# Performance work log

Measured on AMD Instinct MI355X. Metric: run time of the kernel, lower is better.

Reference implementation:

```python
import jax, jax.numpy as jnp
import numpy as np

B, E, U, N = 2, 16, 8, 400
D = E + U  # GP input dim = obs_dim + action_dim


def _psd(key, b, n, scale):
    a = jax.random.normal(key, (b, n, n)) * scale
    return a @ jnp.swapaxes(a, -1, -2) + 1e-4 * jnp.eye(n, dtype=jnp.float32)


def setup_inputs() -> dict:
    key = jax.random.key(0)
    ks = jax.random.split(key, 9)
    X_train = jax.random.normal(ks[0], (N, D), dtype=jnp.float32)
    lengthscales = jax.random.uniform(ks[1], (E, D), minval=0.7, maxval=1.5, dtype=jnp.float32)
    variances = jax.random.uniform(ks[2], (E, 1), minval=0.5, maxval=1.5, dtype=jnp.float32)
    noises = jnp.full((E,), 0.01, dtype=jnp.float32)
    y_train = jax.random.normal(ks[3], (N, E), dtype=jnp.float32) * 0.1

    # cached factorizations, exactly as _extract_parameters builds them
    Xs = X_train[None] / lengthscales[:, None, :]                   # (E,N,D)
    sq = jnp.sum(Xs * Xs, -1)
    d2 = jnp.maximum(sq[:, :, None] + sq[:, None, :] - 2.0 * jnp.einsum('end,emd->enm', Xs, Xs), 0.0)
    K = variances[:, :, None] * jnp.exp(-0.5 * d2)
    K = K + (noises[:, None, None] + 1e-6) * jnp.eye(N, dtype=jnp.float32)
    L = jnp.linalg.cholesky(K)
    inv_K = jax.scipy.linalg.cho_solve((L, True), jnp.broadcast_to(jnp.eye(N, dtype=jnp.float32), (E, N, N)))
    beta = jax.scipy.linalg.cho_solve((L, True), y_train.T[:, :, None])[..., 0]  # (E,N)

    m_x = jax.random.normal(ks[4], (B, E), dtype=jnp.float32)
    m_u = jax.random.normal(ks[5], (B, U), dtype=jnp.float32)
    s_x = _psd(ks[6], B, E, 0.05)
    s_u = _psd(ks[7], B, U, 0.05)
    c_xu = jax.random.normal(ks[8], (B, E, U), dtype=jnp.float32) * 0.1
    return dict(m_x=m_x, s_x=s_x, m_u=m_u, s_u=s_u, c_xu=c_xu,
                X_train=X_train, lengthscales=lengthscales, variances=variances,
                noises=noises, inv_K=inv_K, beta=beta)


def _moment_match(m_x, s_x, m_u, s_u, c_xu, X_train, lengthscales, variances, noises, inv_K, beta):
    Eo = m_x.shape[-1]
    Din = X_train.shape[-1]
    m = jnp.concatenate([m_x, m_u], axis=-1)                        # (B,D) joint input mean
    s_c = s_x @ c_xu                                                # (B,E,U) joint cross block
    S = jnp.concatenate([
        jnp.concatenate([s_x, s_c], axis=-1),
        jnp.concatenate([jnp.swapaxes(s_c, -1, -2), s_u], axis=-1)], axis=-2)  # (B,D,D)

    inp = X_train[None] - m[:, None]                                # (B,N,D)  nu_n = x_n - m
    iL = 1.0 / lengthscales                                         # (E,D)  Lambda^{-1/2}
    iLsq = iL * iL                                                  # (E,D)  Lambda^{-1}
    eyeD = jnp.eye(Din, dtype=m_x.dtype)

    # ---- predictive mean: q_n = s2 |Bm|^{-1/2} exp(-0.5 nu Bm^{-1} nu),  Bm = L^{-1/2} S L^{-1/2} + I
    inv_N = inp[:, None] * iL[None, :, None]                        # (B,E,N,D)
    Bmat = iL[None, :, :, None] * S[:, None] * iL[None, :, None, :] + eyeD  # (B,E,D,D)
    t = jnp.swapaxes(jnp.linalg.solve(Bmat, jnp.swapaxes(inv_N, -1, -2)), -1, -2)  # (B,E,N,D)
    lb = jnp.exp(-0.5 * jnp.sum(inv_N * t, -1)) * beta[None]        # (B,E,N)
    _, logdetB = jnp.linalg.slogdet(Bmat)
    c = variances[:, 0][None] * jnp.exp(-0.5 * logdetB)             # (B,E)
    pred_mean = jnp.sum(lb, -1) * c                                 # (B,E)

    # ---- input-output covariance V (premultiplication by S applied below)
    t_iL = t * iL[None, :, None, :]                                 # rows: nu_n (Lambda + S)^{-1}
    V = jnp.einsum('bend,ben->bde', t_iL, lb) * c[:, None, :]       # (B,D,E)

    # ---- predictive covariance via exact moment matching (PILCO)
    z = inp[:, None] * iLsq[None, :, None]                          # (B,E,N,D) = nu Lambda_a^{-1}
    iLsum = iLsq[:, None] + iLsq[None]                              # (E,E,D)
    R = S[:, None, None] * iLsum[None, :, :, None, :] + eyeD        # (B,E,E,D,D)
    Q2 = 0.5 * jnp.linalg.solve(R, jnp.broadcast_to(S[:, None, None], R.shape))
    Xs = jnp.einsum('band,bacde,bane->bacn', z, Q2, z)              # (B,E,E,N)
    X2s = jnp.einsum('bcnd,bacde,bcne->bacn', z, Q2, z)
    cross = 2.0 * jnp.einsum('baid,bacde,bcje->bacij', z, Q2, z)    # (B,E,E,N,N)
    logk = jnp.log(variances[:, 0])[None, :, None] - 0.5 * jnp.einsum('bnd,ed->ben', inp * inp, iLsq)
    Lmat = jnp.exp(logk[:, :, None, :, None] + logk[:, None, :, None, :]
                   + Xs[..., :, None] + X2s[..., None, :] + cross)  # (B,E,E,N,N)
    _, logdetR = jnp.linalg.slogdet(R)
    scale = jnp.exp(-0.5 * logdetR)                                 # (B,E,E)
    S_bLb = jnp.einsum('ai,bacij,cj->bac', beta, Lmat, beta)
    diagL = Lmat[:, jnp.arange(Eo), jnp.arange(Eo)]                 # (B,E,N,N)
    tr = jnp.einsum('aij,baij->ba', inv_K, diagL)                   # tr(K^{-1} Q_aa)
    eyeE = jnp.eye(Eo, dtype=m_x.dtype)
    S_delta = (S_bLb - eyeE[None] * tr[:, :, None]) * scale \
              + eyeE[None] * variances[:, 0][None, :, None] \
              - pred_mean[:, :, None] * pred_mean[:, None, :]

    # GP predicts the residual delta: next = obs + delta
    next_mean = m_x + pred_mean
    Cx = S[:, :Eo, :] @ V                                           # cov(x, delta), (B,E,E)
    next_var = s_x + S_delta + Cx + jnp.swapaxes(Cx, -1, -2)
    return next_mean, next_var


def reference(m_x, s_x, m_u, s_u, c_xu, X_train, lengthscales, variances, noises, inv_K, beta):
    return _moment_match(m_x, s_x, m_u, s_u, c_xu, X_train, lengthscales, variances, noises, inv_K, beta)
```

## Files before the change

### kernel.cpp

```cpp
#include <hip/hip_runtime.h>
#include <math.h>

#define Bdim 2
#define Edim 16
#define Udim 8
#define Ndim 400
#define Ddim 24
#define NPAIR 136

#define WS_S     0
#define WS_INP   1152
#define WS_LOGK  20352
#define WS_PM    33152
#define WS_V     33184
#define WS_SBLB  33952
#define WS_TR    34464
#define WS_SCALE 34496

__global__ __launch_bounds__(256) void prep_kernel(
    const float* __restrict__ m_x, const float* __restrict__ s_x,
    const float* __restrict__ m_u, const float* __restrict__ s_u,
    const float* __restrict__ c_xu, const float* __restrict__ X_train,
    const float* __restrict__ lengthscales, const float* __restrict__ variances,
    const float* __restrict__ beta, float* __restrict__ ws)
{
    const int b = blockIdx.x / Edim;
    const int e = blockIdx.x % Edim;
    const int t = threadIdx.x;
    const int NT = 256;

    __shared__ float sS[Ddim][Ddim];
    __shared__ float sm[Ddim];
    __shared__ float siL[Ddim], siLsq[Ddim];
    __shared__ float aug[Ddim][2*Ddim];
    __shared__ float fac[Ddim];
    __shared__ float slogdet;
    __shared__ float scv;
    __shared__ float sV[Ddim];
    __shared__ float s_lb;

    if (t < Edim) sm[t] = m_x[b*Edim + t];
    else if (t < Ddim) sm[t] = m_u[b*Udim + (t - Edim)];
    if (t < Ddim) {
        float L = lengthscales[e*Ddim + t];
        siL[t] = 1.f / L;
        siLsq[t] = 1.f / (L*L);
        sV[t] = 0.f;
    }
    if (t == 0) { slogdet = 0.f; s_lb = 0.f; }
    __syncthreads();

    for (int idx = t; idx < Ddim*Ddim; idx += NT) {
        int i = idx / Ddim, j = idx % Ddim;
        float val;
        if (i < Edim && j < Edim) {
            val = s_x[(b*Edim + i)*Edim + j];
        } else if (i >= Edim && j >= Edim) {
            val = s_u[(b*Udim + (i-Edim))*Udim + (j-Edim)];
        } else {
            int r  = (i < Edim) ? i : j;
            int cc = (i < Edim) ? (j - Edim) : (i - Edim);
            float acc = 0.f;
            for (int k = 0; k < Edim; k++)
                acc += s_x[(b*Edim + r)*Edim + k] * c_xu[(b*Edim + k)*Udim + cc];
            val = acc;
        }
        sS[i][j] = val;
        if (e == 0) ws[WS_S + b*Ddim*Ddim + idx] = val;
    }
    __syncthreads();

    for (int idx = t; idx < Ddim*2*Ddim; idx += NT) {
        int i = idx / (2*Ddim), j = idx % (2*Ddim);
        float v;
        if (j < Ddim) v = siL[i]*sS[i][j]*siL[j] + ((i==j) ? 1.f : 0.f);
        else          v = ((j - Ddim) == i) ? 1.f : 0.f;
        aug[i][j] = v;
    }
    __syncthreads();

    for (int k = 0; k < Ddim; k++) {
        float piv = aug[k][k];
        __syncthreads();
        float ipv = 1.f / piv;
        if (t < 2*Ddim) aug[k][t] *= ipv;
        if (t < Ddim) fac[t] = aug[t][k];
        if (t == 0) slogdet += logf(fabsf(piv));
        __syncthreads();
        for (int idx = t; idx < Ddim*2*Ddim; idx += NT) {
            int i = idx / (2*Ddim), j = idx % (2*Ddim);
            if (i != k) aug[i][j] -= fac[i]*aug[k][j];
        }
        __syncthreads();
    }

    if (t == 0) scv = variances[e] * __expf(-0.5f * slogdet);
    __syncthreads();
    const float cval = scv;
    const float logvar = logf(variances[e]);

    float accV[Ddim];
    #pragma unroll
    for (int d = 0; d < Ddim; d++) accV[d] = 0.f;
    float acc_lb = 0.f;

    for (int n = t; n < Ndim; n += NT) {
        float ipv[Ddim], q[Ddim];
        #pragma unroll
        for (int d = 0; d < Ddim; d++) {
            float x = X_train[n*Ddim + d] - sm[d];
            ipv[d] = x;
            q[d] = x * siL[d];
        }
        float tv[Ddim];
        #pragma unroll
        for (int i = 0; i < Ddim; i++) {
            float acc = 0.f;
            #pragma unroll
            for (int j = 0; j < Ddim; j++) acc = fmaf(aug[i][Ddim + j], q[j], acc);
            tv[i] = acc;
        }
        float qt = 0.f, sq2 = 0.f;
        #pragma unroll
        for (int d = 0; d < Ddim; d++) {
            qt  = fmaf(q[d], tv[d], qt);
            sq2 = fmaf(ipv[d]*ipv[d], siLsq[d], sq2);
        }
        float lb = __expf(-0.5f*qt) * beta[e*Ndim + n];
        acc_lb += lb;
        #pragma unroll
        for (int d = 0; d < Ddim; d++) accV[d] = fmaf(tv[d]*siL[d], lb, accV[d]);
        ws[WS_LOGK + (b*Edim + e)*Ndim + n] = logvar - 0.5f*sq2;
        if (e == 0) {
            #pragma unroll
            for (int d = 0; d < Ddim; d++) ws[WS_INP + (b*Ndim + n)*Ddim + d] = ipv[d];
        }
    }
    atomicAdd(&s_lb, acc_lb);
    #pragma unroll
    for (int d = 0; d < Ddim; d++) atomicAdd(&sV[d], accV[d]);
    __syncthreads();
    if (t == 0) ws[WS_PM + b*Edim + e] = cval * s_lb;
    if (t < Ddim) ws[WS_V + (b*Ddim + t)*Edim + e] = cval * sV[t];
}

__global__ __launch_bounds__(512) void main_kernel(
    const float* __restrict__ lengthscales, const float* __restrict__ beta,
    const float* __restrict__ inv_K, float* __restrict__ ws)
{
    const int bid = blockIdx.x;
    const int b = bid / (NPAIR*2);
    const int rem = bid % (NPAIR*2);
    const int pair = rem >> 1;
    const int ih = rem & 1;
    int p = pair, a = 0;
    while (p >= Edim - a) { p -= Edim - a; a++; }
    const int c = a + p;
    const int t = threadIdx.x;
    const int NT = 512;
    const bool diag = (a == c);
    const int cidx = (b*Edim + a)*Edim + c;
    const int ibeg = ih ? 192 : 0;
    const int iend = ih ? Ndim : 192;

    __shared__ float sS[Ddim][Ddim];
    __shared__ float sQ2[Ddim][Ddim];
    __shared__ float aug[Ddim][2*Ddim];
    __shared__ float fac[Ddim];
    __shared__ float sLamA[Ddim], sLamC[Ddim];
    __shared__ float yc[Ndim][28];
    __shared__ float su[Ndim], sv[Ndim], sp[Ndim], sq_[Ndim];
    __shared__ float slogdet, redS, redT;

    if (t < Ddim) {
        float La = lengthscales[a*Ddim + t];
        float Lc = lengthscales[c*Ddim + t];
        sLamA[t] = 1.f/(La*La);
        sLamC[t] = 1.f/(Lc*Lc);
    }
    if (t == 0) { slogdet = 0.f; redS = 0.f; redT = 0.f; }
    for (int idx = t; idx < Ddim*Ddim; idx += NT)
        sS[idx/Ddim][idx%Ddim] = ws[WS_S + b*Ddim*Ddim + idx];
    __syncthreads();

    for (int idx = t; idx < Ddim*2*Ddim; idx += NT) {
        int i = idx/(2*Ddim), j = idx%(2*Ddim);
        float v;
        if (j < Ddim) v = sS[i][j]*(sLamA[j]+sLamC[j]) + ((i==j) ? 1.f : 0.f);
        else          v = sS[i][j-Ddim];
        aug[i][j] = v;
    }
    __syncthreads();
    for (int k = 0; k < Ddim; k++) {
        float piv = aug[k][k];
        __syncthreads();
        float ipv = 1.f/piv;
        if (t < 2*Ddim) aug[k][t] *= ipv;
        if (t < Ddim) fac[t] = aug[t][k];
        if (t == 0) slogdet += logf(fabsf(piv));
        __syncthreads();
        for (int idx = t; idx < Ddim*2*Ddim; idx += NT) {
            int i = idx/(2*Ddim), j = idx%(2*Ddim);
            if (i != k) aug[i][j] -= fac[i]*aug[k][j];
        }
        __syncthreads();
    }
    for (int idx = t; idx < Ddim*Ddim; idx += NT) {
        int i = idx/Ddim, j = idx%Ddim;
        sQ2[i][j] = 0.5f*aug[i][Ddim + j];
    }
    if (t == 0 && ih == 0) ws[WS_SCALE + cidx] = __expf(-0.5f*slogdet);
    __syncthreads();

    if (t < Ndim) {
        int n = t;
        float zav[Ddim], zcv[Ddim];
        #pragma unroll
        for (int d = 0; d < Ddim; d++) {
            float x = ws[WS_INP + (b*Ndim + n)*Ddim + d];
            zav[d] = x * sLamA[d];
            zcv[d] = x * sLamC[d];
        }
        float xs = 0.f, x2s = 0.f;
        #pragma unroll
        for (int i = 0; i < Ddim; i++) {
            float ya = 0.f, ycv = 0.f;
            #pragma unroll
            for (int j = 0; j < Ddim; j++) {
                ya  = fmaf(sQ2[i][j], zav[j], ya);
                ycv = fmaf(sQ2[i][j], zcv[j], ycv);
            }
            xs  = fmaf(zav[i], ya, xs);
            x2s = fmaf(zcv[i], ycv, x2s);
            yc[n][i] = ycv;
        }
        float lka = ws[WS_LOGK + (b*Edim + a)*Ndim + n];
        float lkc = ws[WS_LOGK + (b*Edim + c)*Ndim + n];
        float pa = __expf(lka + xs);
        float qc = __expf(lkc + x2s);
        sp[n] = pa; sq_[n] = qc;
        su[n] = beta[a*Ndim + n]*pa;
        sv[n] = beta[c*Ndim + n]*qc;
    }
    __syncthreads();

    const int tx = t & 15, ty = t >> 4;
    float accS = 0.f, accT = 0.f;
    for (int i0 = ibeg; i0 < iend; i0 += 32) {
        int i = i0 + ty;
        bool iv = (i < iend);
        int isafe = iv ? i : ibeg;
        float zr[Ddim];
        #pragma unroll
        for (int d = 0; d < Ddim; d++)
            zr[d] = ws[WS_INP + (b*Ndim + isafe)*Ddim + d] * sLamA[d];
        float ui = iv ? su[i] : 0.f;
        float pi = (iv && diag) ? sp[i] : 0.f;
        const float* kr = &inv_K[((size_t)a*Ndim + isafe)*Ndim];
        for (int j0 = 0; j0 < Ndim; j0 += 16) {
            int j = j0 + tx;
            float dt = 0.f;
            #pragma unroll
            for (int d = 0; d < Ddim; d++) dt = fmaf(zr[d], yc[j][d], dt);
            float ex = __expf(2.f*dt);
            accS = fmaf(ui*sv[j], ex, accS);
            if (diag) accT = fmaf(pi*sq_[j]*kr[j], ex, accT);
        }
    }
    atomicAdd(&redS, accS);
    if (diag) atomicAdd(&redT, accT);
    __syncthreads();
    if (t == 0) {
        atomicAdd(&ws[WS_SBLB + cidx], redS);
        if (diag) atomicAdd(&ws[WS_TR + b*Edim + a], redT);
    }
}

__global__ __launch_bounds__(256) void final_kernel(
    const float* __restrict__ m_x, const float* __restrict__ s_x,
    const float* __restrict__ variances, const float* __restrict__ ws,
    float* __restrict__ out)
{
    const int b = blockIdx.x;
    const int t = threadIdx.x;
    if (t < Edim) out[b*Edim + t] = m_x[b*Edim + t] + ws[WS_PM + b*Edim + t];
    const int i = t >> 4, j = t & 15;
    const int lo = (i < j) ? i : j;
    const int hi = (i < j) ? j : i;
    float pmi = ws[WS_PM + b*Edim + i], pmj = ws[WS_PM + b*Edim + j];
    float cxij = 0.f, cxji = 0.f;
    #pragma unroll
    for (int d = 0; d < Ddim; d++) {
        cxij += ws[WS_S + b*Ddim*Ddim + i*Ddim + d]*ws[WS_V + (b*Ddim + d)*Edim + j];
        cxji += ws[WS_S + b*Ddim*Ddim + j*Ddim + d]*ws[WS_V + (b*Ddim + d)*Edim + i];
    }
    float sb  = ws[WS_SBLB + (b*Edim + lo)*Edim + hi];
    float scl = ws[WS_SCALE + (b*Edim + lo)*Edim + hi];
    float sd = sb;
    if (i == j) sd -= ws[WS_TR + b*Edim + i];
    sd = sd*scl + ((i==j) ? variances[i] : 0.f) - pmi*pmj;
    out[Bdim*Edim + (b*Edim + i)*Edim + j] = s_x[(b*Edim + i)*Edim + j] + sd + cxij + cxji;
}

extern "C" void kernel_launch(void* const* d_in, const int* in_sizes, int n_in,
                              void* d_out, int out_size, void* d_ws, size_t ws_size,
                              hipStream_t stream) {
    const float* m_x     = (const float*)d_in[0];
    const float* s_x     = (const float*)d_in[1];
    const float* m_u     = (const float*)d_in[2];
    const float* s_u     = (const float*)d_in[3];
    const float* c_xu    = (const float*)d_in[4];
    const float* X_train = (const float*)d_in[5];
    const float* ls      = (const float*)d_in[6];
    const float* var     = (const float*)d_in[7];
    const float* inv_K   = (const float*)d_in[9];
    const float* beta    = (const float*)d_in[10];
    float* ws  = (float*)d_ws;
    float* out = (float*)d_out;

    hipMemsetAsync(ws + WS_SBLB, 0, (Bdim*Edim*Edim + Bdim*Edim)*sizeof(float), stream);

    hipLaunchKernelGGL(prep_kernel, dim3(Bdim*Edim), dim3(256), 0, stream,
        m_x, s_x, m_u, s_u, c_xu, X_train, ls, var, beta, ws);
    hipLaunchKernelGGL(main_kernel, dim3(Bdim*NPAIR*2), dim3(512), 0, stream,
        ls, beta, inv_K, ws);
    hipLaunchKernelGGL(final_kernel, dim3(Bdim), dim3(256), 0, stream,
        m_x, s_x, var, ws, out);
}
```

Before: 332.7 us.

## Compute all ordered (a,c) pairs per block, drop atomics, memset and row split

The main kernel now launches one block for every ordered (a,c) output pair, 512 blocks in all. Before, it used two half-row blocks for each of the 136 symmetric pairs, which also made 544 blocks. Each block now covers all 400 rows and writes its result directly, so the global atomics and the workspace memset go away, and the final kernel reads entries without mapping to the upper triangle. The cost is redundant work: the symmetric lower-triangle pairs are recomputed, including their 24x24 inversions. A launch-bounds occupancy hint of 4 blocks per CU is also added.

```diff
diff --git a/kernel.cpp b/kernel.cpp
--- a/kernel.cpp
+++ b/kernel.cpp
@@ -6,7 +6,6 @@
 #define Udim 8
 #define Ndim 400
 #define Ddim 24
-#define NPAIR 136
 
 #define WS_S     0
 #define WS_INP   1152
@@ -144,24 +143,17 @@
     if (t < Ddim) ws[WS_V + (b*Ddim + t)*Edim + e] = cval * sV[t];
 }
 
-__global__ __launch_bounds__(512) void main_kernel(
+__global__ __launch_bounds__(512, 4) void main_kernel(
     const float* __restrict__ lengthscales, const float* __restrict__ beta,
     const float* __restrict__ inv_K, float* __restrict__ ws)
 {
     const int bid = blockIdx.x;
-    const int b = bid / (NPAIR*2);
-    const int rem = bid % (NPAIR*2);
-    const int pair = rem >> 1;
-    const int ih = rem & 1;
-    int p = pair, a = 0;
-    while (p >= Edim - a) { p -= Edim - a; a++; }
-    const int c = a + p;
+    const int b = bid / (Edim*Edim);
+    const int a = (bid / Edim) % Edim;
+    const int c = bid % Edim;
     const int t = threadIdx.x;
     const int NT = 512;
     const bool diag = (a == c);
-    const int cidx = (b*Edim + a)*Edim + c;
-    const int ibeg = ih ? 192 : 0;
-    const int iend = ih ? Ndim : 192;
 
     __shared__ float sS[Ddim][Ddim];
     __shared__ float sQ2[Ddim][Ddim];
@@ -209,7 +201,7 @@
         int i = idx/Ddim, j = idx%Ddim;
         sQ2[i][j] = 0.5f*aug[i][Ddim + j];
     }
-    if (t == 0 && ih == 0) ws[WS_SCALE + cidx] = __expf(-0.5f*slogdet);
+    if (t == 0) ws[WS_SCALE + bid] = __expf(-0.5f*slogdet);
     __syncthreads();
 
     if (t < Ndim) {
@@ -246,10 +238,10 @@
 
     const int tx = t & 15, ty = t >> 4;
     float accS = 0.f, accT = 0.f;
-    for (int i0 = ibeg; i0 < iend; i0 += 32) {
+    for (int i0 = 0; i0 < Ndim; i0 += 32) {
         int i = i0 + ty;
-        bool iv = (i < iend);
-        int isafe = iv ? i : ibeg;
+        bool iv = (i < Ndim);
+        int isafe = iv ? i : 0;
         float zr[Ddim];
         #pragma unroll
         for (int d = 0; d < Ddim; d++)
@@ -271,8 +263,8 @@
     if (diag) atomicAdd(&redT, accT);
     __syncthreads();
     if (t == 0) {
-        atomicAdd(&ws[WS_SBLB + cidx], redS);
-        if (diag) atomicAdd(&ws[WS_TR + b*Edim + a], redT);
+        ws[WS_SBLB + bid] = redS;
+        if (diag) ws[WS_TR + b*Edim + a] = redT;
     }
 }
 
@@ -285,8 +277,6 @@
     const int t = threadIdx.x;
     if (t < Edim) out[b*Edim + t] = m_x[b*Edim + t] + ws[WS_PM + b*Edim + t];
     const int i = t >> 4, j = t & 15;
-    const int lo = (i < j) ? i : j;
-    const int hi = (i < j) ? j : i;
     float pmi = ws[WS_PM + b*Edim + i], pmj = ws[WS_PM + b*Edim + j];
     float cxij = 0.f, cxji = 0.f;
     #pragma unroll
@@ -294,8 +284,8 @@
         cxij += ws[WS_S + b*Ddim*Ddim + i*Ddim + d]*ws[WS_V + (b*Ddim + d)*Edim + j];
         cxji += ws[WS_S + b*Ddim*Ddim + j*Ddim + d]*ws[WS_V + (b*Ddim + d)*Edim + i];
     }
-    float sb  = ws[WS_SBLB + (b*Edim + lo)*Edim + hi];
-    float scl = ws[WS_SCALE + (b*Edim + lo)*Edim + hi];
+    float sb  = ws[WS_SBLB + (b*Edim + i)*Edim + j];
+    float scl = ws[WS_SCALE + (b*Edim + i)*Edim + j];
     float sd = sb;
     if (i == j) sd -= ws[WS_TR + b*Edim + i];
     sd = sd*scl + ((i==j) ? variances[i] : 0.f) - pmi*pmj;
@@ -318,11 +308,9 @@
     float* ws  = (float*)d_ws;
     float* out = (float*)d_out;
 
-    hipMemsetAsync(ws + WS_SBLB, 0, (Bdim*Edim*Edim + Bdim*Edim)*sizeof(float), stream);
-
     hipLaunchKernelGGL(prep_kernel, dim3(Bdim*Edim), dim3(256), 0, stream,
         m_x, s_x, m_u, s_u, c_xu, X_train, ls, var, beta, ws);
-    hipLaunchKernelGGL(main_kernel, dim3(Bdim*NPAIR*2), dim3(512), 0, stream,
+    hipLaunchKernelGGL(main_kernel, dim3(Bdim*Edim*Edim), dim3(512), 0, stream,
         ls, beta, inv_K, ws);
     hipLaunchKernelGGL(final_kernel, dim3(Bdim), dim3(256), 0, stream,
         m_x, s_x, var, ws, out);
```

New measurement: 378.4 us. 13.8% more time.
